# Optimization experiments

Measured on AMD Instinct MI355X. Metric: run time of the kernel, lower is better.

## Reference

```python
import jax, jax.numpy as jnp
import numpy as np

N_NODES = 50000
N_EDGES = 800000

def _sage_conv(x, src, dst, W, b, n_nodes):
    # DGL SAGEConv aggregator_type='gcn':
    #   h_neigh = (sum_{u in N(v)} x_u + x_v) / (in_deg(v) + 1)
    #   out = h_neigh @ W.T + b   (fc_self unused for gcn aggregator)
    agg = jax.ops.segment_sum(x[src], dst, num_segments=n_nodes)  # [N, d]
    deg = jax.ops.segment_sum(jnp.ones((src.shape[0],), x.dtype), dst, num_segments=n_nodes)
    h = (agg + x) / (deg + 1.0)[:, None]
    return h @ W.T + b

def setup_inputs() -> dict:
    key = jax.random.key(0)
    ks = jax.random.split(key, 9)
    d_in, d_hid, d_out = 128, 128, 64
    x = jax.random.normal(ks[0], (N_NODES, d_in), dtype=jnp.float32)
    src = jax.random.randint(ks[1], (N_EDGES,), 0, N_NODES, dtype=jnp.int32)
    dst = jax.random.randint(ks[2], (N_EDGES,), 0, N_NODES, dtype=jnp.int32)
    def glorot(k, shape):
        fan = shape[0] + shape[1]
        return jax.random.normal(k, shape, dtype=jnp.float32) * jnp.sqrt(2.0 / fan)
    W1 = glorot(ks[3], (d_hid, d_in))
    b1 = jnp.zeros((d_hid,), jnp.float32)
    W2 = glorot(ks[4], (d_hid, d_hid))
    b2 = jnp.zeros((d_hid,), jnp.float32)
    W3 = glorot(ks[5], (d_out, d_hid))
    b3 = jnp.zeros((d_out,), jnp.float32)
    return {"x": x, "src": src, "dst": dst, "W1": W1, "b1": b1,
            "W2": W2, "b2": b2, "W3": W3, "b3": b3}

def reference(x, src, dst, W1, b1, W2, b2, W3, b3):
    n = x.shape[0]
    h = jax.nn.relu(_sage_conv(x, src, dst, W1, b1, n))
    h = jax.nn.relu(_sage_conv(h, src, dst, W2, b2, n))
    h = jax.nn.sigmoid(_sage_conv(h, src, dst, W3, b3, n))
    return h
```

## Files before the change

### kernel.cpp

```cpp
#include <hip/hip_runtime.h>
#include <hip/hip_bf16.h>
#include <math.h>


#define NFEAT 128
#define BSH   7
#define NBUKP 512
#define EPB   2048
#define BCAP  3072

typedef __attribute__((ext_vector_type(8))) short bf16x8;
typedef __attribute__((ext_vector_type(4))) float f32x4;

__device__ __forceinline__ unsigned short f2bf(float f) {
    unsigned u = __float_as_uint(f);
    u += 0x7fffu + ((u >> 16) & 1u);
    return (unsigned short)(u >> 16);
}
__device__ __forceinline__ float bflo(unsigned u) { return __uint_as_float(u << 16); }
__device__ __forceinline__ float bfhi(unsigned u) { return __uint_as_float(u & 0xffff0000u); }


__global__ __launch_bounds__(256) void partA1_count(const int* __restrict__ dst,
                                                    int* __restrict__ bucketCnt, int E) {
    __shared__ int hist[NBUKP];
    const int t = threadIdx.x;
    hist[t] = 0; hist[t + 256] = 0;
    __syncthreads();
    const int base = blockIdx.x * EPB;
#pragma unroll
    for (int j = 0; j < EPB / 256; ++j) {
        int e = base + t + 256 * j;
        if (e < E) atomicAdd(&hist[dst[e] >> BSH], 1);
    }
    __syncthreads();
    for (int b = t; b < NBUKP; b += 256) {
        int h = hist[b];
        if (h > 0) atomicAdd(&bucketCnt[b], h);
    }
}


__global__ __launch_bounds__(512) void partA2_scan(const int* __restrict__ bucketCnt,
                                                   int* __restrict__ bucketOff,
                                                   int* __restrict__ bucketCursor,
                                                   int* __restrict__ row_ptr, int N, int E) {
    __shared__ int sc[NBUKP];
    const int t = threadIdx.x;
    sc[t] = bucketCnt[t];
    __syncthreads();
    for (int off = 1; off < NBUKP; off <<= 1) {
        int v = (t >= off) ? sc[t - off] : 0;
        __syncthreads();
        sc[t] += v;
        __syncthreads();
    }
    int excl = sc[t] - bucketCnt[t];
    bucketOff[t] = excl;
    bucketCursor[t] = excl;
    if (t == 0) row_ptr[N] = E;
}


__global__ __launch_bounds__(256) void partA3_scatter(const int* __restrict__ src,
                                                      const int* __restrict__ dst,
                                                      int* __restrict__ bucketCursor,
                                                      unsigned long long* __restrict__ pairs,
                                                      int E) {
    __shared__ int hist[NBUKP];
    __shared__ int sc[NBUKP];
    __shared__ int lcur[NBUKP];
    __shared__ int lbase[NBUKP];
    __shared__ unsigned long long stage[EPB];
    __shared__ int destIdx[EPB];
    __shared__ int nLocalSh;

    const int t = threadIdx.x;
    hist[t] = 0; hist[t + 256] = 0;
    lcur[t] = 0; lcur[t + 256] = 0;
    __syncthreads();

    const int base = blockIdx.x * EPB;
    int bb[EPB / 256];
    unsigned long long pr[EPB / 256];
#pragma unroll
    for (int j = 0; j < EPB / 256; ++j) {
        int e = base + t + 256 * j;
        bb[j] = -1;
        if (e < E) {
            int s = src[e], d = dst[e];
            int b = d >> BSH;
            bb[j] = b;
            pr[j] = ((unsigned long long)(unsigned)d << 32) | (unsigned)s;
            atomicAdd(&hist[b], 1);
        }
    }
    __syncthreads();
    sc[t] = hist[t]; sc[t + 256] = hist[t + 256];
    __syncthreads();
    for (int off = 1; off < NBUKP; off <<= 1) {
        int v0 = (t >= off) ? sc[t - off] : 0;
        int v1 = (t + 256 >= off) ? sc[t + 256 - off] : 0;
        __syncthreads();
        sc[t] += v0; sc[t + 256] += v1;
        __syncthreads();
    }
    if (t == 255) nLocalSh = sc[NBUKP - 1];
    sc[t] -= hist[t]; sc[t + 256] -= hist[t + 256];
    for (int b = t; b < NBUKP; b += 256) {
        int h = hist[b];
        if (h > 0) lbase[b] = atomicAdd(&bucketCursor[b], h);
    }
    __syncthreads();
#pragma unroll
    for (int j = 0; j < EPB / 256; ++j) {
        int b = bb[j];
        if (b >= 0) {
            int slot = atomicAdd(&lcur[b], 1);
            int spos = sc[b] + slot;
            stage[spos] = pr[j];
            destIdx[spos] = lbase[b] + slot;
        }
    }
    __syncthreads();
    const int nLocal = nLocalSh;
#pragma unroll
    for (int j = 0; j < EPB / 256; ++j) {
        int i = t + 256 * j;
        if (i < nLocal) pairs[destIdx[i]] = stage[i];
    }
}


__global__ __launch_bounds__(256) void partB_build(const unsigned long long* __restrict__ pairs,
                                                   const int* __restrict__ bucketOff,
                                                   const int* __restrict__ bucketCnt,
                                                   int* __restrict__ row_ptr,
                                                   float* __restrict__ deg_inv,
                                                   int* __restrict__ col_idx, int N) {
    __shared__ unsigned long long pairsL[BCAP];
    __shared__ int srcS[BCAP];
    __shared__ int nhist[128];
    __shared__ int npref[128];
    __shared__ int ncur[128];

    const int t = threadIdx.x;
    const int b = blockIdx.x;
    const int nodeBase = b << BSH;
    const int eBeg = bucketOff[b];
    const int eCnt = bucketCnt[b];

    if (t < 128) { nhist[t] = 0; ncur[t] = 0; }
    __syncthreads();

    if (eCnt <= BCAP) {
        for (int i = t; i < eCnt; i += 256) {
            unsigned long long p = pairs[eBeg + i];
            pairsL[i] = p;
            atomicAdd(&nhist[(int)(p >> 32) - nodeBase], 1);
        }
        __syncthreads();
        if (t < 128) npref[t] = nhist[t];
        __syncthreads();
        for (int off = 1; off < 128; off <<= 1) {
            int v = (t < 128 && t >= off) ? npref[t - off] : 0;
            __syncthreads();
            if (t < 128) npref[t] += v;
            __syncthreads();
        }
        if (t < 128) npref[t] -= nhist[t];
        if (t < 128 && nodeBase + t < N) {
            row_ptr[nodeBase + t] = eBeg + npref[t];
            deg_inv[nodeBase + t] = 1.0f / (float)(nhist[t] + 1);
        }
        __syncthreads();
        for (int i = t; i < eCnt; i += 256) {
            unsigned long long p = pairsL[i];
            int d = (int)(p >> 32) - nodeBase;
            int slot = atomicAdd(&ncur[d], 1);
            srcS[npref[d] + slot] = (int)(unsigned)p;
        }
        __syncthreads();
        for (int i = t; i < eCnt; i += 256) col_idx[eBeg + i] = srcS[i];
    } else {
        for (int i = t; i < eCnt; i += 256) {
            unsigned long long p = pairs[eBeg + i];
            atomicAdd(&nhist[(int)(p >> 32) - nodeBase], 1);
        }
        __syncthreads();
        if (t < 128) npref[t] = nhist[t];
        __syncthreads();
        for (int off = 1; off < 128; off <<= 1) {
            int v = (t < 128 && t >= off) ? npref[t - off] : 0;
            __syncthreads();
            if (t < 128) npref[t] += v;
            __syncthreads();
        }
        if (t < 128) npref[t] -= nhist[t];
        if (t < 128 && nodeBase + t < N) {
            row_ptr[nodeBase + t] = eBeg + npref[t];
            deg_inv[nodeBase + t] = 1.0f / (float)(nhist[t] + 1);
        }
        __syncthreads();
        for (int i = t; i < eCnt; i += 256) {
            unsigned long long p = pairs[eBeg + i];
            int d = (int)(p >> 32) - nodeBase;
            int slot = atomicAdd(&ncur[d], 1);
            col_idx[eBeg + npref[d] + slot] = (int)(unsigned)p;
        }
    }
}


__global__ __launch_bounds__(256) void cvt_bf16_kernel(const float* __restrict__ in,
                                                       ushort* __restrict__ outb, int n4) {
    int i = blockIdx.x * blockDim.x + threadIdx.x;
    if (i < n4) {
        float4 f = *(const float4*)(in + (size_t)i * 4);
        ushort4 u = make_ushort4(f2bf(f.x), f2bf(f.y), f2bf(f.z), f2bf(f.w));
        *(ushort4*)(outb + (size_t)i * 4) = u;
    }
}

__global__ __launch_bounds__(256) void cvt_weights_kernel(const float* __restrict__ W1,
                                                          const float* __restrict__ W2,
                                                          const float* __restrict__ W3,
                                                          ushort* __restrict__ w1,
                                                          ushort* __restrict__ w2,
                                                          ushort* __restrict__ w3,
                                                          int n1, int n2, int n3) {
    int i = blockIdx.x * blockDim.x + threadIdx.x;
    const float* src; ushort* dst; int off;
    if (i < n1)            { src = W1; dst = w1; off = i; }
    else if (i < n1 + n2)  { src = W2; dst = w2; off = i - n1; }
    else if (i < n1+n2+n3) { src = W3; dst = w3; off = i - n1 - n2; }
    else return;
    float4 f = *(const float4*)(src + (size_t)off * 4);
    *(ushort4*)(dst + (size_t)off * 4) = make_ushort4(f2bf(f.x), f2bf(f.y), f2bf(f.z), f2bf(f.w));
}


template<int SECOND>
__global__ __launch_bounds__(256) void fused_agg_gemm_kernel(
        const ushort* __restrict__ Xb,
        const int* __restrict__ row_ptr,
        const int* __restrict__ col_idx,
        const float* __restrict__ deg_inv,
        const ushort* __restrict__ Wb,
        const float* __restrict__ bias,
        const ushort* __restrict__ W3b,
        ushort* __restrict__ outB, int N) {
    __shared__ ushort A[16][136];
    __shared__ ushort H2[SECOND ? 16 : 1][136];

    const int t    = threadIdx.x;
    const int w    = t >> 6;
    const int lane = t & 63;
    const int base = blockIdx.x * 16;
    const unsigned* Xu = (const unsigned*)Xb;

#pragma unroll
    for (int i = 0; i < 4; ++i) {
        const int v = base + w * 4 + i;
        if (v < N) {
            const int beg = row_ptr[v];
            const int end = row_ptr[v + 1];
            const int deg = end - beg;
            int cidx = 0;
            if (lane < deg) cidx = col_idx[beg + lane];

            float a0 = 0.f, a1 = 0.f, b0 = 0.f, b1 = 0.f;
            float c0 = 0.f, c1 = 0.f, d0 = 0.f, d1 = 0.f;
            const int nfast = deg < 64 ? deg : 64;
            int j = 0;
            for (; j + 3 < nfast; j += 4) {
                int s0 = __shfl(cidx, j + 0, 64);
                int s1 = __shfl(cidx, j + 1, 64);
                int s2 = __shfl(cidx, j + 2, 64);
                int s3 = __shfl(cidx, j + 3, 64);
                unsigned u0 = Xu[(size_t)s0 * 64 + lane];
                unsigned u1 = Xu[(size_t)s1 * 64 + lane];
                unsigned u2 = Xu[(size_t)s2 * 64 + lane];
                unsigned u3 = Xu[(size_t)s3 * 64 + lane];
                a0 += bflo(u0); a1 += bfhi(u0);
                b0 += bflo(u1); b1 += bfhi(u1);
                c0 += bflo(u2); c1 += bfhi(u2);
                d0 += bflo(u3); d1 += bfhi(u3);
            }
            for (; j < nfast; ++j) {
                int s0 = __shfl(cidx, j, 64);
                unsigned u0 = Xu[(size_t)s0 * 64 + lane];
                a0 += bflo(u0); a1 += bfhi(u0);
            }
            for (int e = beg + 64; e < end; ++e) {
                unsigned u0 = Xu[(size_t)col_idx[e] * 64 + lane];
                a0 += bflo(u0); a1 += bfhi(u0);
            }
            unsigned us = Xu[(size_t)v * 64 + lane];
            float inv = deg_inv[v];
            float r0 = (a0 + b0 + c0 + d0 + bflo(us)) * inv;
            float r1 = (a1 + b1 + c1 + d1 + bfhi(us)) * inv;
            unsigned ru = (unsigned)f2bf(r0) | ((unsigned)f2bf(r1) << 16);
            ((unsigned*)&A[w * 4 + i][0])[lane] = ru;
        }
    }
    __syncthreads();

    const int m    = lane & 15;
    const int quad = lane >> 4;
    f32x4 acc0 = {0.f, 0.f, 0.f, 0.f};
    f32x4 acc1 = {0.f, 0.f, 0.f, 0.f};
    {
        const ushort* arow = &A[m][quad * 8];
        const ushort* wrow = Wb + (size_t)(w * 32 + m) * NFEAT + quad * 8;
#pragma unroll
        for (int k0 = 0; k0 < NFEAT; k0 += 32) {
            bf16x8 a  = *(const bf16x8*)(arow + k0);
            bf16x8 bA = *(const bf16x8*)(wrow + k0);
            bf16x8 bB = *(const bf16x8*)(wrow + 16 * NFEAT + k0);
            acc0 = __builtin_amdgcn_mfma_f32_16x16x32_bf16(a, bA, acc0, 0, 0, 0);
            acc1 = __builtin_amdgcn_mfma_f32_16x16x32_bf16(a, bB, acc1, 0, 0, 0);
        }
    }
    const float bv0 = bias[w * 32 + m];
    const float bv1 = bias[w * 32 + 16 + m];

    if (!SECOND) {
#pragma unroll
        for (int r = 0; r < 4; ++r) {
            int row = base + quad * 4 + r;
            if (row < N) {
                outB[(size_t)row * NFEAT + w * 32 + m]      = f2bf(fmaxf(acc0[r] + bv0, 0.f));
                outB[(size_t)row * NFEAT + w * 32 + 16 + m] = f2bf(fmaxf(acc1[r] + bv1, 0.f));
            }
        }
    } else {
#pragma unroll
        for (int r = 0; r < 4; ++r) {
            H2[quad * 4 + r][w * 32 + m]      = f2bf(fmaxf(acc0[r] + bv0, 0.f));
            H2[quad * 4 + r][w * 32 + 16 + m] = f2bf(fmaxf(acc1[r] + bv1, 0.f));
        }
        __syncthreads();
        f32x4 acc3 = {0.f, 0.f, 0.f, 0.f};
        const ushort* hrow  = &H2[m][quad * 8];
        const ushort* w3row = W3b + (size_t)(w * 16 + m) * NFEAT + quad * 8;
#pragma unroll
        for (int k0 = 0; k0 < NFEAT; k0 += 32) {
            bf16x8 a = *(const bf16x8*)(hrow + k0);
            bf16x8 b = *(const bf16x8*)(w3row + k0);
            acc3 = __builtin_amdgcn_mfma_f32_16x16x32_bf16(a, b, acc3, 0, 0, 0);
        }
#pragma unroll
        for (int r = 0; r < 4; ++r) {
            int row = base + quad * 4 + r;
            if (row < N) outB[(size_t)row * 64 + w * 16 + m] = f2bf(acc3[r]);
        }
    }
}


__global__ __launch_bounds__(256) void agg64_sigmoid_kernel(const ushort* __restrict__ Gb,
                                                            const int* __restrict__ row_ptr,
                                                            const int* __restrict__ col_idx,
                                                            const float* __restrict__ deg_inv,
                                                            const float* __restrict__ bias,
                                                            float* __restrict__ out, int N) {
    const int wp   = blockIdx.x * (blockDim.x >> 6) + (threadIdx.x >> 6);
    const int lane = threadIdx.x & 63;
    const int half = lane >> 5;
    const int hl   = lane & 31;
    const int v    = wp * 2 + half;
    const bool act = (v < N);

    int beg = 0, end = 0;
    if (act) { beg = row_ptr[v]; end = row_ptr[v + 1]; }
    const int deg = end - beg;
    const unsigned* Gu = (const unsigned*)Gb;

    int cidx = 0;
    if (hl < deg) cidx = col_idx[beg + hl];

    float a0 = 0.f, a1 = 0.f, b0 = 0.f, b1 = 0.f;
    float c0 = 0.f, c1 = 0.f, d0 = 0.f, d1 = 0.f;
    const int nfast = deg < 32 ? deg : 32;
    int j = 0;
    for (; j + 3 < nfast; j += 4) {
        int s0 = __shfl(cidx, j + 0, 32);
        int s1 = __shfl(cidx, j + 1, 32);
        int s2 = __shfl(cidx, j + 2, 32);
        int s3 = __shfl(cidx, j + 3, 32);
        unsigned u0 = Gu[(size_t)s0 * 32 + hl];
        unsigned u1 = Gu[(size_t)s1 * 32 + hl];
        unsigned u2 = Gu[(size_t)s2 * 32 + hl];
        unsigned u3 = Gu[(size_t)s3 * 32 + hl];
        a0 += bflo(u0); a1 += bfhi(u0);
        b0 += bflo(u1); b1 += bfhi(u1);
        c0 += bflo(u2); c1 += bfhi(u2);
        d0 += bflo(u3); d1 += bfhi(u3);
    }
    for (; j < nfast; ++j) {
        int s0 = __shfl(cidx, j, 32);
        unsigned u0 = Gu[(size_t)s0 * 32 + hl];
        a0 += bflo(u0); a1 += bfhi(u0);
    }
    for (int e = beg + 32; e < end; ++e) {
        unsigned u0 = Gu[(size_t)col_idx[e] * 32 + hl];
        a0 += bflo(u0); a1 += bfhi(u0);
    }
    if (act) {
        unsigned us = Gu[(size_t)v * 32 + hl];
        float inv = deg_inv[v];
        float r0 = (a0 + b0 + c0 + d0 + bflo(us)) * inv + bias[hl * 2 + 0];
        float r1 = (a1 + b1 + c1 + d1 + bfhi(us)) * inv + bias[hl * 2 + 1];
        r0 = 1.0f / (1.0f + __expf(-r0));
        r1 = 1.0f / (1.0f + __expf(-r1));
        *(float2*)(out + (size_t)v * 64 + hl * 2) = make_float2(r0, r1);
    }
}


static inline size_t align256(size_t x) { return (x + 255) & ~(size_t)255; }

extern "C" void kernel_launch(void* const* d_in, const int* in_sizes, int n_in,
                              void* d_out, int out_size, void* d_ws, size_t ws_size,
                              hipStream_t stream) {
    const float* x   = (const float*)d_in[0];
    const int*   src = (const int*)d_in[1];
    const int*   dst = (const int*)d_in[2];
    const float* W1  = (const float*)d_in[3];
    const float* b1  = (const float*)d_in[4];
    const float* W2  = (const float*)d_in[5];
    const float* b2  = (const float*)d_in[6];
    const float* W3  = (const float*)d_in[7];
    const float* b3  = (const float*)d_in[8];
    float*       out = (float*)d_out;

    const int N = in_sizes[0] / NFEAT;
    const int E = in_sizes[1];
    const int D_OUT = in_sizes[7] / NFEAT;
    const int NBUK = (N + (1 << BSH) - 1) >> BSH;
    const int PBLK = (E + EPB - 1) / EPB;

    char* ws = (char*)d_ws;
    int* row_ptr      = (int*)ws;  ws += align256((size_t)(N + 1) * 4);
    int* col_idx      = (int*)ws;  ws += align256((size_t)E * 4);
    float* deg_inv    = (float*)ws; ws += align256((size_t)N * 4);
    int* bucketCnt    = (int*)ws;  ws += align256((size_t)NBUKP * 4);
    int* bucketOff    = (int*)ws;  ws += align256((size_t)NBUKP * 4);
    int* bucketCursor = (int*)ws;  ws += align256((size_t)NBUKP * 4);
    ushort* w1bf      = (ushort*)ws; ws += align256((size_t)NFEAT * NFEAT * 2);
    ushort* w2bf      = (ushort*)ws; ws += align256((size_t)NFEAT * NFEAT * 2);
    ushort* w3bf      = (ushort*)ws; ws += align256((size_t)D_OUT * NFEAT * 2);
    ushort* xbf       = (ushort*)ws; ws += align256((size_t)N * NFEAT * 2);
    ushort* h1bf      = (ushort*)ws; ws += align256((size_t)N * NFEAT * 2);
    ushort* gbf = xbf;
    unsigned long long* pairs = (unsigned long long*)h1bf;

    hipMemsetAsync(bucketCnt, 0, (size_t)NBUKP * 4, stream);
    partA1_count<<<PBLK, 256, 0, stream>>>(dst, bucketCnt, E);
    partA2_scan<<<1, NBUKP, 0, stream>>>(bucketCnt, bucketOff, bucketCursor, row_ptr, N, E);
    partA3_scatter<<<PBLK, 256, 0, stream>>>(src, dst, bucketCursor, pairs, E);
    partB_build<<<NBUK, 256, 0, stream>>>(pairs, bucketOff, bucketCnt, row_ptr, deg_inv, col_idx, N);

    const int n4 = N * NFEAT / 4;
    cvt_bf16_kernel<<<(n4 + 255) / 256, 256, 0, stream>>>(x, xbf, n4);
    const int n1 = NFEAT * NFEAT / 4, n2 = NFEAT * NFEAT / 4, n3 = D_OUT * NFEAT / 4;
    cvt_weights_kernel<<<(n1 + n2 + n3 + 255) / 256, 256, 0, stream>>>(
        W1, W2, W3, w1bf, w2bf, w3bf, n1, n2, n3);

    const int fusedBlocks = (N + 15) / 16;
    const int agg64Blocks = (N + 7) / 8;

    fused_agg_gemm_kernel<0><<<fusedBlocks, 256, 0, stream>>>(
        xbf, row_ptr, col_idx, deg_inv, w1bf, b1, nullptr, h1bf, N);
    fused_agg_gemm_kernel<1><<<fusedBlocks, 256, 0, stream>>>(
        h1bf, row_ptr, col_idx, deg_inv, w2bf, b2, w3bf, gbf, N);
    agg64_sigmoid_kernel<<<agg64Blocks, 256, 0, stream>>>(gbf, row_ptr, col_idx, deg_inv, b3, out, N);
}
```

Measured before the change: 241.6 us.

## Split features into 32-column planes and separate aggregation from MFMA GEMMs

```diff
diff --git a/kernel.cpp b/kernel.cpp
--- a/kernel.cpp
+++ b/kernel.cpp
@@ -212,14 +212,17 @@
 }
 
 
-__global__ __launch_bounds__(256) void cvt_bf16_kernel(const float* __restrict__ in,
-                                                       ushort* __restrict__ outb, int n4) {
+__global__ __launch_bounds__(256) void cvt_x_planes_kernel(const float* __restrict__ in,
+                                                           ushort* __restrict__ outp, int N) {
     int i = blockIdx.x * blockDim.x + threadIdx.x;
-    if (i < n4) {
-        float4 f = *(const float4*)(in + (size_t)i * 4);
-        ushort4 u = make_ushort4(f2bf(f.x), f2bf(f.y), f2bf(f.z), f2bf(f.w));
-        *(ushort4*)(outb + (size_t)i * 4) = u;
-    }
+    if (i >= N * 32) return;
+    int node = i >> 5;
+    int f0   = (i & 31) * 4;
+    int p    = f0 >> 5;
+    int c    = f0 & 31;
+    float4 f = *(const float4*)(in + (size_t)node * NFEAT + f0);
+    *(ushort4*)(outp + ((size_t)p * N + node) * 32 + c) =
+        make_ushort4(f2bf(f.x), f2bf(f.y), f2bf(f.z), f2bf(f.w));
 }
 
 __global__ __launch_bounds__(256) void cvt_weights_kernel(const float* __restrict__ W1,
@@ -240,69 +243,134 @@
 }
 
 
-template<int SECOND>
-__global__ __launch_bounds__(256) void fused_agg_gemm_kernel(
-        const ushort* __restrict__ Xb,
+template<int PL, int SIG>
+__global__ __launch_bounds__(256) void agg_plane_kernel(
+        const ushort* __restrict__ Xpl,
         const int* __restrict__ row_ptr,
         const int* __restrict__ col_idx,
         const float* __restrict__ deg_inv,
-        const ushort* __restrict__ Wb,
         const float* __restrict__ bias,
-        const ushort* __restrict__ W3b,
-        ushort* __restrict__ outB, int N) {
+        ushort* __restrict__ outB,
+        float* __restrict__ outF, int N) {
+    const int s    = blockIdx.x % PL;
+    const int tile = blockIdx.x / PL;
+    const int w    = threadIdx.x >> 6;
+    const int lane = threadIdx.x & 63;
+    const int g    = lane >> 4;
+    const int f    = lane & 15;
+    const unsigned* P = (const unsigned*)Xpl + (size_t)s * N * 16;
+
+#pragma unroll
+    for (int i = 0; i < 4; ++i) {
+        const int v = tile * 16 + w * 4 + i;
+        if (v >= N) continue;
+        const int beg = row_ptr[v];
+        const int end = row_ptr[v + 1];
+
+        float a0 = 0.f, a1 = 0.f, b0 = 0.f, b1 = 0.f;
+        int e = beg + g;
+        for (; e + 4 < end; e += 8) {
+            int s0 = col_idx[e];
+            int s1 = col_idx[e + 4];
+            unsigned u0 = P[(size_t)s0 * 16 + f];
+            unsigned u1 = P[(size_t)s1 * 16 + f];
+            a0 += bflo(u0); a1 += bfhi(u0);
+            b0 += bflo(u1); b1 += bfhi(u1);
+        }
+        if (e < end) {
+            unsigned u0 = P[(size_t)col_idx[e] * 16 + f];
+            a0 += bflo(u0); a1 += bfhi(u0);
+        }
+        a0 += b0; a1 += b1;
+        a0 += __shfl_xor(a0, 16, 64); a0 += __shfl_xor(a0, 32, 64);
+        a1 += __shfl_xor(a1, 16, 64); a1 += __shfl_xor(a1, 32, 64);
+        if (g == 0) {
+            unsigned us = P[(size_t)v * 16 + f];
+            float inv = deg_inv[v];
+            float r0 = (a0 + bflo(us)) * inv;
+            float r1 = (a1 + bfhi(us)) * inv;
+            if (!SIG) {
+                ((unsigned*)outB)[(size_t)v * (PL * 16) + s * 16 + f] =
+                    (unsigned)f2bf(r0) | ((unsigned)f2bf(r1) << 16);
+            } else {
+                r0 += bias[s * 32 + 2 * f + 0];
+                r1 += bias[s * 32 + 2 * f + 1];
+                r0 = 1.0f / (1.0f + __expf(-r0));
+                r1 = 1.0f / (1.0f + __expf(-r1));
+                *(float2*)(outF + (size_t)v * 64 + s * 32 + 2 * f) = make_float2(r0, r1);
+            }
+        }
+    }
+}
+
+
+template<int NCT, int PLANE_OUT>
+__global__ __launch_bounds__(256) void gemm_mfma_kernel(const ushort* __restrict__ Hb,
+                                                        const ushort* __restrict__ Wb,
+                                                        const float* __restrict__ bias,
+                                                        ushort* __restrict__ outB,
+                                                        int N, int relu) {
+    const int OUT  = NCT * 16;
+    const int wid  = blockIdx.x * 4 + (threadIdx.x >> 6);
+    const int lane = threadIdx.x & 63;
+    const int m    = lane & 15;
+    const int quad = lane >> 4;
+    const int row0 = wid * 16;
+    if (row0 >= N) return;
+
+    f32x4 acc[NCT];
+#pragma unroll
+    for (int i = 0; i < NCT; ++i) acc[i] = (f32x4){0.f, 0.f, 0.f, 0.f};
+
+    const ushort* hrow = Hb + (size_t)(row0 + m) * NFEAT + quad * 8;
+    const ushort* wrow = Wb + (size_t)m * NFEAT + quad * 8;
+
+#pragma unroll
+    for (int k0 = 0; k0 < NFEAT; k0 += 32) {
+        bf16x8 a = *(const bf16x8*)(hrow + k0);
+#pragma unroll
+        for (int ct = 0; ct < NCT; ++ct) {
+            bf16x8 b = *(const bf16x8*)(wrow + (size_t)ct * 16 * NFEAT + k0);
+            acc[ct] = __builtin_amdgcn_mfma_f32_16x16x32_bf16(a, b, acc[ct], 0, 0, 0);
+        }
+    }
+
+#pragma unroll
+    for (int ct = 0; ct < NCT; ++ct) {
+        float bv = bias ? bias[ct * 16 + m] : 0.f;
+#pragma unroll
+        for (int r = 0; r < 4; ++r) {
+            float v = acc[ct][r] + bv;
+            if (relu) v = fmaxf(v, 0.f);
+            int row = row0 + quad * 4 + r;
+            if (PLANE_OUT) {
+                outB[((size_t)(ct >> 1) * N + row) * 32 + (ct & 1) * 16 + m] = f2bf(v);
+            } else {
+                outB[(size_t)row * OUT + ct * 16 + m] = f2bf(v);
+            }
+        }
+    }
+}
+
+
+__global__ __launch_bounds__(256) void gemm23_kernel(const ushort* __restrict__ Ab,
+                                                     const ushort* __restrict__ W2b,
+                                                     const float* __restrict__ b2,
+                                                     const ushort* __restrict__ W3b,
+                                                     ushort* __restrict__ outP, int N) {
     __shared__ ushort A[16][136];
-    __shared__ ushort H2[SECOND ? 16 : 1][136];
-
+    __shared__ ushort H2[16][136];
     const int t    = threadIdx.x;
     const int w    = t >> 6;
     const int lane = t & 63;
     const int base = blockIdx.x * 16;
-    const unsigned* Xu = (const unsigned*)Xb;
-
-#pragma unroll
-    for (int i = 0; i < 4; ++i) {
-        const int v = base + w * 4 + i;
-        if (v < N) {
-            const int beg = row_ptr[v];
-            const int end = row_ptr[v + 1];
-            const int deg = end - beg;
-            int cidx = 0;
-            if (lane < deg) cidx = col_idx[beg + lane];
-
-            float a0 = 0.f, a1 = 0.f, b0 = 0.f, b1 = 0.f;
-            float c0 = 0.f, c1 = 0.f, d0 = 0.f, d1 = 0.f;
-            const int nfast = deg < 64 ? deg : 64;
-            int j = 0;
-            for (; j + 3 < nfast; j += 4) {
-                int s0 = __shfl(cidx, j + 0, 64);
-                int s1 = __shfl(cidx, j + 1, 64);
-                int s2 = __shfl(cidx, j + 2, 64);
-                int s3 = __shfl(cidx, j + 3, 64);
-                unsigned u0 = Xu[(size_t)s0 * 64 + lane];
-                unsigned u1 = Xu[(size_t)s1 * 64 + lane];
-                unsigned u2 = Xu[(size_t)s2 * 64 + lane];
-                unsigned u3 = Xu[(size_t)s3 * 64 + lane];
-                a0 += bflo(u0); a1 += bfhi(u0);
-                b0 += bflo(u1); b1 += bfhi(u1);
-                c0 += bflo(u2); c1 += bfhi(u2);
-                d0 += bflo(u3); d1 += bfhi(u3);
-            }
-            for (; j < nfast; ++j) {
-                int s0 = __shfl(cidx, j, 64);
-                unsigned u0 = Xu[(size_t)s0 * 64 + lane];
-                a0 += bflo(u0); a1 += bfhi(u0);
-            }
-            for (int e = beg + 64; e < end; ++e) {
-                unsigned u0 = Xu[(size_t)col_idx[e] * 64 + lane];
-                a0 += bflo(u0); a1 += bfhi(u0);
-            }
-            unsigned us = Xu[(size_t)v * 64 + lane];
-            float inv = deg_inv[v];
-            float r0 = (a0 + b0 + c0 + d0 + bflo(us)) * inv;
-            float r1 = (a1 + b1 + c1 + d1 + bfhi(us)) * inv;
-            unsigned ru = (unsigned)f2bf(r0) | ((unsigned)f2bf(r1) << 16);
-            ((unsigned*)&A[w * 4 + i][0])[lane] = ru;
-        }
+
+    {
+        const int r  = t >> 4;
+        const int c8 = (t & 15) * 8;
+        bf16x8 av = {};
+        if (base + r < N) av = *(const bf16x8*)(Ab + (size_t)(base + r) * NFEAT + c8);
+        *(bf16x8*)&A[r][c8] = av;
     }
     __syncthreads();
 
@@ -312,7 +380,7 @@
     f32x4 acc1 = {0.f, 0.f, 0.f, 0.f};
     {
         const ushort* arow = &A[m][quad * 8];
-        const ushort* wrow = Wb + (size_t)(w * 32 + m) * NFEAT + quad * 8;
+        const ushort* wrow = W2b + (size_t)(w * 32 + m) * NFEAT + quad * 8;
 #pragma unroll
         for (int k0 = 0; k0 < NFEAT; k0 += 32) {
             bf16x8 a  = *(const bf16x8*)(arow + k0);
@@ -322,99 +390,28 @@
             acc1 = __builtin_amdgcn_mfma_f32_16x16x32_bf16(a, bB, acc1, 0, 0, 0);
         }
     }
-    const float bv0 = bias[w * 32 + m];
-    const float bv1 = bias[w * 32 + 16 + m];
-
-    if (!SECOND) {
-#pragma unroll
-        for (int r = 0; r < 4; ++r) {
-            int row = base + quad * 4 + r;
-            if (row < N) {
-                outB[(size_t)row * NFEAT + w * 32 + m]      = f2bf(fmaxf(acc0[r] + bv0, 0.f));
-                outB[(size_t)row * NFEAT + w * 32 + 16 + m] = f2bf(fmaxf(acc1[r] + bv1, 0.f));
-            }
-        }
-    } else {
-#pragma unroll
-        for (int r = 0; r < 4; ++r) {
-            H2[quad * 4 + r][w * 32 + m]      = f2bf(fmaxf(acc0[r] + bv0, 0.f));
-            H2[quad * 4 + r][w * 32 + 16 + m] = f2bf(fmaxf(acc1[r] + bv1, 0.f));
-        }
-        __syncthreads();
-        f32x4 acc3 = {0.f, 0.f, 0.f, 0.f};
-        const ushort* hrow  = &H2[m][quad * 8];
-        const ushort* w3row = W3b + (size_t)(w * 16 + m) * NFEAT + quad * 8;
-#pragma unroll
-        for (int k0 = 0; k0 < NFEAT; k0 += 32) {
-            bf16x8 a = *(const bf16x8*)(hrow + k0);
-            bf16x8 b = *(const bf16x8*)(w3row + k0);
-            acc3 = __builtin_amdgcn_mfma_f32_16x16x32_bf16(a, b, acc3, 0, 0, 0);
-        }
-#pragma unroll
-        for (int r = 0; r < 4; ++r) {
-            int row = base + quad * 4 + r;
-            if (row < N) outB[(size_t)row * 64 + w * 16 + m] = f2bf(acc3[r]);
-        }
-    }
-}
-
-
-__global__ __launch_bounds__(256) void agg64_sigmoid_kernel(const ushort* __restrict__ Gb,
-                                                            const int* __restrict__ row_ptr,
-                                                            const int* __restrict__ col_idx,
-                                                            const float* __restrict__ deg_inv,
-                                                            const float* __restrict__ bias,
-                                                            float* __restrict__ out, int N) {
-    const int wp   = blockIdx.x * (blockDim.x >> 6) + (threadIdx.x >> 6);
-    const int lane = threadIdx.x & 63;
-    const int half = lane >> 5;
-    const int hl   = lane & 31;
-    const int v    = wp * 2 + half;
-    const bool act = (v < N);
-
-    int beg = 0, end = 0;
-    if (act) { beg = row_ptr[v]; end = row_ptr[v + 1]; }
-    const int deg = end - beg;
-    const unsigned* Gu = (const unsigned*)Gb;
-
-    int cidx = 0;
-    if (hl < deg) cidx = col_idx[beg + hl];
-
-    float a0 = 0.f, a1 = 0.f, b0 = 0.f, b1 = 0.f;
-    float c0 = 0.f, c1 = 0.f, d0 = 0.f, d1 = 0.f;
-    const int nfast = deg < 32 ? deg : 32;
-    int j = 0;
-    for (; j + 3 < nfast; j += 4) {
-        int s0 = __shfl(cidx, j + 0, 32);
-        int s1 = __shfl(cidx, j + 1, 32);
-        int s2 = __shfl(cidx, j + 2, 32);
-        int s3 = __shfl(cidx, j + 3, 32);
-        unsigned u0 = Gu[(size_t)s0 * 32 + hl];
-        unsigned u1 = Gu[(size_t)s1 * 32 + hl];
-        unsigned u2 = Gu[(size_t)s2 * 32 + hl];
-        unsigned u3 = Gu[(size_t)s3 * 32 + hl];
-        a0 += bflo(u0); a1 += bfhi(u0);
-        b0 += bflo(u1); b1 += bfhi(u1);
-        c0 += bflo(u2); c1 += bfhi(u2);
-        d0 += bflo(u3); d1 += bfhi(u3);
-    }
-    for (; j < nfast; ++j) {
-        int s0 = __shfl(cidx, j, 32);
-        unsigned u0 = Gu[(size_t)s0 * 32 + hl];
-        a0 += bflo(u0); a1 += bfhi(u0);
-    }
-    for (int e = beg + 32; e < end; ++e) {
-        unsigned u0 = Gu[(size_t)col_idx[e] * 32 + hl];
-        a0 += bflo(u0); a1 += bfhi(u0);
-    }
-    if (act) {
-        unsigned us = Gu[(size_t)v * 32 + hl];
-        float inv = deg_inv[v];
-        float r0 = (a0 + b0 + c0 + d0 + bflo(us)) * inv + bias[hl * 2 + 0];
-        float r1 = (a1 + b1 + c1 + d1 + bfhi(us)) * inv + bias[hl * 2 + 1];
-        r0 = 1.0f / (1.0f + __expf(-r0));
-        r1 = 1.0f / (1.0f + __expf(-r1));
-        *(float2*)(out + (size_t)v * 64 + hl * 2) = make_float2(r0, r1);
+    const float bv0 = b2[w * 32 + m];
+    const float bv1 = b2[w * 32 + 16 + m];
+#pragma unroll
+    for (int r = 0; r < 4; ++r) {
+        H2[quad * 4 + r][w * 32 + m]      = f2bf(fmaxf(acc0[r] + bv0, 0.f));
+        H2[quad * 4 + r][w * 32 + 16 + m] = f2bf(fmaxf(acc1[r] + bv1, 0.f));
+    }
+    __syncthreads();
+    f32x4 acc3 = {0.f, 0.f, 0.f, 0.f};
+    const ushort* hrow  = &H2[m][quad * 8];
+    const ushort* w3row = W3b + (size_t)(w * 16 + m) * NFEAT + quad * 8;
+#pragma unroll
+    for (int k0 = 0; k0 < NFEAT; k0 += 32) {
+        bf16x8 a = *(const bf16x8*)(hrow + k0);
+        bf16x8 b = *(const bf16x8*)(w3row + k0);
+        acc3 = __builtin_amdgcn_mfma_f32_16x16x32_bf16(a, b, acc3, 0, 0, 0);
+    }
+#pragma unroll
+    for (int r = 0; r < 4; ++r) {
+        int row = base + quad * 4 + r;
+        if (row < N)
+            outP[((size_t)(w >> 1) * N + row) * 32 + (w & 1) * 16 + m] = f2bf(acc3[r]);
     }
 }
 
@@ -451,10 +448,11 @@
     ushort* w1bf      = (ushort*)ws; ws += align256((size_t)NFEAT * NFEAT * 2);
     ushort* w2bf      = (ushort*)ws; ws += align256((size_t)NFEAT * NFEAT * 2);
     ushort* w3bf      = (ushort*)ws; ws += align256((size_t)D_OUT * NFEAT * 2);
-    ushort* xbf       = (ushort*)ws; ws += align256((size_t)N * NFEAT * 2);
-    ushort* h1bf      = (ushort*)ws; ws += align256((size_t)N * NFEAT * 2);
-    ushort* gbf = xbf;
-    unsigned long long* pairs = (unsigned long long*)h1bf;
+    ushort* xpl       = (ushort*)ws; ws += align256((size_t)N * NFEAT * 2);
+    ushort* h1pl      = (ushort*)ws; ws += align256((size_t)N * NFEAT * 2);
+    ushort* aggB      = (ushort*)ws; ws += align256((size_t)N * NFEAT * 2);
+    ushort* gpl = xpl;
+    unsigned long long* pairs = (unsigned long long*)h1pl;
 
     hipMemsetAsync(bucketCnt, 0, (size_t)NBUKP * 4, stream);
     partA1_count<<<PBLK, 256, 0, stream>>>(dst, bucketCnt, E);
@@ -462,18 +460,20 @@
     partA3_scatter<<<PBLK, 256, 0, stream>>>(src, dst, bucketCursor, pairs, E);
     partB_build<<<NBUK, 256, 0, stream>>>(pairs, bucketOff, bucketCnt, row_ptr, deg_inv, col_idx, N);
 
-    const int n4 = N * NFEAT / 4;
-    cvt_bf16_kernel<<<(n4 + 255) / 256, 256, 0, stream>>>(x, xbf, n4);
+    cvt_x_planes_kernel<<<(N * 32 + 255) / 256, 256, 0, stream>>>(x, xpl, N);
     const int n1 = NFEAT * NFEAT / 4, n2 = NFEAT * NFEAT / 4, n3 = D_OUT * NFEAT / 4;
     cvt_weights_kernel<<<(n1 + n2 + n3 + 255) / 256, 256, 0, stream>>>(
         W1, W2, W3, w1bf, w2bf, w3bf, n1, n2, n3);
 
-    const int fusedBlocks = (N + 15) / 16;
-    const int agg64Blocks = (N + 7) / 8;
-
-    fused_agg_gemm_kernel<0><<<fusedBlocks, 256, 0, stream>>>(
-        xbf, row_ptr, col_idx, deg_inv, w1bf, b1, nullptr, h1bf, N);
-    fused_agg_gemm_kernel<1><<<fusedBlocks, 256, 0, stream>>>(
-        h1bf, row_ptr, col_idx, deg_inv, w2bf, b2, w3bf, gbf, N);
-    agg64_sigmoid_kernel<<<agg64Blocks, 256, 0, stream>>>(gbf, row_ptr, col_idx, deg_inv, b3, out, N);
-}
+    const int tiles      = (N + 15) / 16;
+    const int gemmBlocks = (N / 16 + 3) / 4;
+
+    agg_plane_kernel<4, 0><<<tiles * 4, 256, 0, stream>>>(
+        xpl, row_ptr, col_idx, deg_inv, nullptr, aggB, nullptr, N);
+    gemm_mfma_kernel<8, 1><<<gemmBlocks, 256, 0, stream>>>(aggB, w1bf, b1, h1pl, N, 1);
+    agg_plane_kernel<4, 0><<<tiles * 4, 256, 0, stream>>>(
+        h1pl, row_ptr, col_idx, deg_inv, nullptr, aggB, nullptr, N);
+    gemm23_kernel<<<tiles, 256, 0, stream>>>(aggB, w2bf, b2, w3bf, gpl, N);
+    agg_plane_kernel<2, 1><<<tiles * 2, 256, 0, stream>>>(
+        gpl, row_ptr, col_idx, deg_inv, b3, nullptr, out, N);
+}
```

Result: slower. 346.1 us (+43.3%).

## Gather neighbor rows with wide vector loads split across lane groups

Applied to the files above, without the earlier changes.

```diff
diff --git a/kernel.cpp b/kernel.cpp
--- a/kernel.cpp
+++ b/kernel.cpp
@@ -240,6 +240,12 @@
 }
 
 
+#define ACC8(u)                                                     \
+    a0 += bflo((u).x); a1 += bfhi((u).x);                           \
+    a2 += bflo((u).y); a3 += bfhi((u).y);                           \
+    a4 += bflo((u).z); a5 += bfhi((u).z);                           \
+    a6 += bflo((u).w); a7 += bfhi((u).w);
+
 template<int SECOND>
 __global__ __launch_bounds__(256) void fused_agg_gemm_kernel(
         const ushort* __restrict__ Xb,
@@ -256,8 +262,10 @@
     const int t    = threadIdx.x;
     const int w    = t >> 6;
     const int lane = t & 63;
+    const int g    = lane >> 4;
+    const int f    = lane & 15;
     const int base = blockIdx.x * 16;
-    const unsigned* Xu = (const unsigned*)Xb;
+    const uint4* X4 = (const uint4*)Xb;
 
 #pragma unroll
     for (int i = 0; i < 4; ++i) {
@@ -265,43 +273,43 @@
         if (v < N) {
             const int beg = row_ptr[v];
             const int end = row_ptr[v + 1];
-            const int deg = end - beg;
-            int cidx = 0;
-            if (lane < deg) cidx = col_idx[beg + lane];
-
-            float a0 = 0.f, a1 = 0.f, b0 = 0.f, b1 = 0.f;
-            float c0 = 0.f, c1 = 0.f, d0 = 0.f, d1 = 0.f;
-            const int nfast = deg < 64 ? deg : 64;
-            int j = 0;
-            for (; j + 3 < nfast; j += 4) {
-                int s0 = __shfl(cidx, j + 0, 64);
-                int s1 = __shfl(cidx, j + 1, 64);
-                int s2 = __shfl(cidx, j + 2, 64);
-                int s3 = __shfl(cidx, j + 3, 64);
-                unsigned u0 = Xu[(size_t)s0 * 64 + lane];
-                unsigned u1 = Xu[(size_t)s1 * 64 + lane];
-                unsigned u2 = Xu[(size_t)s2 * 64 + lane];
-                unsigned u3 = Xu[(size_t)s3 * 64 + lane];
-                a0 += bflo(u0); a1 += bfhi(u0);
-                b0 += bflo(u1); b1 += bfhi(u1);
-                c0 += bflo(u2); c1 += bfhi(u2);
-                d0 += bflo(u3); d1 += bfhi(u3);
+
+            float a0 = 0.f, a1 = 0.f, a2 = 0.f, a3 = 0.f;
+            float a4 = 0.f, a5 = 0.f, a6 = 0.f, a7 = 0.f;
+            int e = beg + g;
+            for (; e + 12 < end; e += 16) {
+                int s0 = col_idx[e];
+                int s1 = col_idx[e + 4];
+                int s2 = col_idx[e + 8];
+                int s3 = col_idx[e + 12];
+                uint4 u0 = X4[(size_t)s0 * 16 + f];
+                uint4 u1 = X4[(size_t)s1 * 16 + f];
+                uint4 u2 = X4[(size_t)s2 * 16 + f];
+                uint4 u3 = X4[(size_t)s3 * 16 + f];
+                ACC8(u0); ACC8(u1); ACC8(u2); ACC8(u3);
             }
-            for (; j < nfast; ++j) {
-                int s0 = __shfl(cidx, j, 64);
-                unsigned u0 = Xu[(size_t)s0 * 64 + lane];
-                a0 += bflo(u0); a1 += bfhi(u0);
+            for (; e < end; e += 4) {
+                uint4 u = X4[(size_t)col_idx[e] * 16 + f];
+                ACC8(u);
             }
-            for (int e = beg + 64; e < end; ++e) {
-                unsigned u0 = Xu[(size_t)col_idx[e] * 64 + lane];
-                a0 += bflo(u0); a1 += bfhi(u0);
+            a0 += __shfl_xor(a0, 16, 64); a0 += __shfl_xor(a0, 32, 64);
+            a1 += __shfl_xor(a1, 16, 64); a1 += __shfl_xor(a1, 32, 64);
+            a2 += __shfl_xor(a2, 16, 64); a2 += __shfl_xor(a2, 32, 64);
+            a3 += __shfl_xor(a3, 16, 64); a3 += __shfl_xor(a3, 32, 64);
+            a4 += __shfl_xor(a4, 16, 64); a4 += __shfl_xor(a4, 32, 64);
+            a5 += __shfl_xor(a5, 16, 64); a5 += __shfl_xor(a5, 32, 64);
+            a6 += __shfl_xor(a6, 16, 64); a6 += __shfl_xor(a6, 32, 64);
+            a7 += __shfl_xor(a7, 16, 64); a7 += __shfl_xor(a7, 32, 64);
+            if (g == 0) {
+                uint4 us = X4[(size_t)v * 16 + f];
+                float inv = deg_inv[v];
+                uint4 r;
+                r.x = (unsigned)f2bf((a0 + bflo(us.x)) * inv) | ((unsigned)f2bf((a1 + bfhi(us.x)) * inv) << 16);
+                r.y = (unsigned)f2bf((a2 + bflo(us.y)) * inv) | ((unsigned)f2bf((a3 + bfhi(us.y)) * inv) << 16);
+                r.z = (unsigned)f2bf((a4 + bflo(us.z)) * inv) | ((unsigned)f2bf((a5 + bfhi(us.z)) * inv) << 16);
+                r.w = (unsigned)f2bf((a6 + bflo(us.w)) * inv) | ((unsigned)f2bf((a7 + bfhi(us.w)) * inv) << 16);
+                ((uint4*)&A[w * 4 + i][0])[f] = r;
             }
-            unsigned us = Xu[(size_t)v * 64 + lane];
-            float inv = deg_inv[v];
-            float r0 = (a0 + b0 + c0 + d0 + bflo(us)) * inv;
-            float r1 = (a1 + b1 + c1 + d1 + bfhi(us)) * inv;
-            unsigned ru = (unsigned)f2bf(r0) | ((unsigned)f2bf(r1) << 16);
-            ((unsigned*)&A[w * 4 + i][0])[lane] = ru;
         }
     }
     __syncthreads();
@@ -365,56 +373,52 @@
                                                             const float* __restrict__ deg_inv,
                                                             const float* __restrict__ bias,
                                                             float* __restrict__ out, int N) {
-    const int wp   = blockIdx.x * (blockDim.x >> 6) + (threadIdx.x >> 6);
+    const int v    = blockIdx.x * (blockDim.x >> 6) + (threadIdx.x >> 6);
     const int lane = threadIdx.x & 63;
-    const int half = lane >> 5;
-    const int hl   = lane & 31;
-    const int v    = wp * 2 + half;
-    const bool act = (v < N);
-
-    int beg = 0, end = 0;
-    if (act) { beg = row_ptr[v]; end = row_ptr[v + 1]; }
-    const int deg = end - beg;
-    const unsigned* Gu = (const unsigned*)Gb;
-
-    int cidx = 0;
-    if (hl < deg) cidx = col_idx[beg + hl];
-
-    float a0 = 0.f, a1 = 0.f, b0 = 0.f, b1 = 0.f;
-    float c0 = 0.f, c1 = 0.f, d0 = 0.f, d1 = 0.f;
-    const int nfast = deg < 32 ? deg : 32;
-    int j = 0;
-    for (; j + 3 < nfast; j += 4) {
-        int s0 = __shfl(cidx, j + 0, 32);
-        int s1 = __shfl(cidx, j + 1, 32);
-        int s2 = __shfl(cidx, j + 2, 32);
-        int s3 = __shfl(cidx, j + 3, 32);
-        unsigned u0 = Gu[(size_t)s0 * 32 + hl];
-        unsigned u1 = Gu[(size_t)s1 * 32 + hl];
-        unsigned u2 = Gu[(size_t)s2 * 32 + hl];
-        unsigned u3 = Gu[(size_t)s3 * 32 + hl];
-        a0 += bflo(u0); a1 += bfhi(u0);
-        b0 += bflo(u1); b1 += bfhi(u1);
-        c0 += bflo(u2); c1 += bfhi(u2);
-        d0 += bflo(u3); d1 += bfhi(u3);
-    }
-    for (; j < nfast; ++j) {
-        int s0 = __shfl(cidx, j, 32);
-        unsigned u0 = Gu[(size_t)s0 * 32 + hl];
-        a0 += bflo(u0); a1 += bfhi(u0);
-    }
-    for (int e = beg + 32; e < end; ++e) {
-        unsigned u0 = Gu[(size_t)col_idx[e] * 32 + hl];
-        a0 += bflo(u0); a1 += bfhi(u0);
-    }
-    if (act) {
-        unsigned us = Gu[(size_t)v * 32 + hl];
+    const int g    = lane >> 4;
+    const int f    = lane & 15;
+    if (v >= N) return;
+    const int beg = row_ptr[v];
+    const int end = row_ptr[v + 1];
+    const uint2* G2 = (const uint2*)Gb;
+
+    float a0 = 0.f, a1 = 0.f, a2 = 0.f, a3 = 0.f;
+    int e = beg + g;
+    for (; e + 12 < end; e += 16) {
+        int s0 = col_idx[e];
+        int s1 = col_idx[e + 4];
+        int s2 = col_idx[e + 8];
+        int s3 = col_idx[e + 12];
+        uint2 u0 = G2[(size_t)s0 * 16 + f];
+        uint2 u1 = G2[(size_t)s1 * 16 + f];
+        uint2 u2 = G2[(size_t)s2 * 16 + f];
+        uint2 u3 = G2[(size_t)s3 * 16 + f];
+        a0 += bflo(u0.x); a1 += bfhi(u0.x); a2 += bflo(u0.y); a3 += bfhi(u0.y);
+        a0 += bflo(u1.x); a1 += bfhi(u1.x); a2 += bflo(u1.y); a3 += bfhi(u1.y);
+        a0 += bflo(u2.x); a1 += bfhi(u2.x); a2 += bflo(u2.y); a3 += bfhi(u2.y);
+        a0 += bflo(u3.x); a1 += bfhi(u3.x); a2 += bflo(u3.y); a3 += bfhi(u3.y);
+    }
+    for (; e < end; e += 4) {
+        uint2 u = G2[(size_t)col_idx[e] * 16 + f];
+        a0 += bflo(u.x); a1 += bfhi(u.x); a2 += bflo(u.y); a3 += bfhi(u.y);
+    }
+    a0 += __shfl_xor(a0, 16, 64); a0 += __shfl_xor(a0, 32, 64);
+    a1 += __shfl_xor(a1, 16, 64); a1 += __shfl_xor(a1, 32, 64);
+    a2 += __shfl_xor(a2, 16, 64); a2 += __shfl_xor(a2, 32, 64);
+    a3 += __shfl_xor(a3, 16, 64); a3 += __shfl_xor(a3, 32, 64);
+    if (g == 0) {
+        uint2 us = G2[(size_t)v * 16 + f];
         float inv = deg_inv[v];
-        float r0 = (a0 + b0 + c0 + d0 + bflo(us)) * inv + bias[hl * 2 + 0];
-        float r1 = (a1 + b1 + c1 + d1 + bfhi(us)) * inv + bias[hl * 2 + 1];
-        r0 = 1.0f / (1.0f + __expf(-r0));
-        r1 = 1.0f / (1.0f + __expf(-r1));
-        *(float2*)(out + (size_t)v * 64 + hl * 2) = make_float2(r0, r1);
+        float4 r;
+        r.x = (a0 + bflo(us.x)) * inv + bias[f * 4 + 0];
+        r.y = (a1 + bfhi(us.x)) * inv + bias[f * 4 + 1];
+        r.z = (a2 + bflo(us.y)) * inv + bias[f * 4 + 2];
+        r.w = (a3 + bfhi(us.y)) * inv + bias[f * 4 + 3];
+        r.x = 1.0f / (1.0f + __expf(-r.x));
+        r.y = 1.0f / (1.0f + __expf(-r.y));
+        r.z = 1.0f / (1.0f + __expf(-r.z));
+        r.w = 1.0f / (1.0f + __expf(-r.w));
+        *(float4*)(out + (size_t)v * 64 + f * 4) = r;
     }
 }
 
@@ -469,7 +473,7 @@
         W1, W2, W3, w1bf, w2bf, w3bf, n1, n2, n3);
 
     const int fusedBlocks = (N + 15) / 16;
-    const int agg64Blocks = (N + 7) / 8;
+    const int agg64Blocks = (N + 3) / 4;
 
     fused_agg_gemm_kernel<0><<<fusedBlocks, 256, 0, stream>>>(
         xbf, row_ptr, col_idx, deg_inv, w1bf, b1, nullptr, h1bf, N);
```

Result: slower. 249.3 us (+3.2%).
